# Performance work log

Hardware: AMD Instinct MI355X
Metric: run time of the kernel (lower is better)

Reference implementation:

```python
import jax, jax.numpy as jnp
import numpy as np

B = 16384
D = 64            # bottom_mlp_layers[-1] = embedding_dim
DENSE = 512
HIST = 50         # history length per row
C_CAMP = 1000     # num_collisions for campaign table (sqrt(1e6))
C_FEAT = 316      # num_collisions for 1e5-vocab tables
NQ_CAMP = 1000    # ceil(1e6/1000)
NQ_FEAT = 317     # ceil(1e5/316)
NFEAT = 7
N = NFEAT + 1 + 1 # sparse features + dense row
PROJ = 128


def setup_inputs() -> dict:
    key = jax.random.key(0)
    ks = jax.random.split(key, 20)
    inp = {
        'x': jax.random.normal(ks[0], (B, DENSE), jnp.float32),
        'hist_idx': jax.random.randint(ks[1], (B * HIST,), 0, 1000000),
        'hist_offsets': jnp.arange(B, dtype=jnp.int64) * HIST,
        'feat_idx': jax.random.randint(ks[2], (B, NFEAT), 0, 100000),
        # QR embedding tables (quotient, remainder)
        'Wq_c': jax.random.normal(ks[3], (NQ_CAMP, D), jnp.float32) * 0.05,
        'Wr_c': jax.random.normal(ks[4], (C_CAMP, D), jnp.float32) * 0.05,
        'Wq_f': jax.random.normal(ks[5], (NFEAT, NQ_FEAT, D), jnp.float32) * 0.05,
        'Wr_f': jax.random.normal(ks[6], (NFEAT, C_FEAT, D), jnp.float32) * 0.05,
        # bottom MLP: 512->512 relu 512->256 relu 256->64
        'W0': jax.random.normal(ks[7], (512, DENSE), jnp.float32) * 0.03,
        'b0': jnp.zeros((512,), jnp.float32),
        'W1': jax.random.normal(ks[8], (256, 512), jnp.float32) * 0.04,
        'b1': jnp.zeros((256,), jnp.float32),
        'W2': jax.random.normal(ks[9], (64, 256), jnp.float32) * 0.06,
        'b2': jnp.zeros((64,), jnp.float32),
        # projection: (D + (N^2-N)/2) -> PROJ ; 64 + 36 = 100
        'Wp': jax.random.normal(ks[10], (PROJ, D + (N * N - N) // 2), jnp.float32) * 0.1,
        'bp': jnp.zeros((PROJ,), jnp.float32),
    }
    return inp


def _forward(x, hist_idx, hist_offsets, feat_idx, Wq_c, Wr_c, Wq_f, Wr_f,
             W0, b0, W1, b1, W2, b2, Wp, bp):
    # bottom MLP
    h = jax.nn.relu(x @ W0.T + b0)
    h = jax.nn.relu(h @ W1.T + b1)
    dense = h @ W2.T + b2                                   # [B, D]

    # QR embedding bag (mode='mean', operation='mult') for history feature
    e = Wq_c[hist_idx // C_CAMP] * Wr_c[hist_idx % C_CAMP]  # [M, D]
    M = hist_idx.shape[0]
    seg = jnp.cumsum(jnp.zeros((M,), jnp.int32).at[hist_offsets].add(1)) - 1
    sums = jax.ops.segment_sum(e, seg, num_segments=B)      # [B, D]
    counts = jnp.diff(jnp.concatenate([hist_offsets, jnp.array([M], hist_offsets.dtype)]))
    hist_emb = sums / counts[:, None].astype(sums.dtype)

    # single-valued QR lookups (bag size 1 -> mean == lookup)
    t = jnp.arange(NFEAT)[None, :]
    fe = Wq_f[t, feat_idx // C_FEAT] * Wr_f[t, feat_idx % C_FEAT]  # [B, NFEAT, D]

    # pairwise dot interaction: upper triangle (offset=1) of T @ T^T
    T = jnp.concatenate([dense[:, None, :], hist_emb[:, None, :], fe], axis=1)  # [B, N, D]
    Z = jnp.einsum('bnd,bmd->bnm', T, T)
    row, col = np.triu_indices(N, k=1)
    Z_flat = Z[:, row, col]                                  # [B, (N^2-N)/2]

    combined = jnp.concatenate([dense, Z_flat], axis=1)
    return combined @ Wp.T + bp                              # [B, PROJ]


def reference(x, hist_idx, hist_offsets, feat_idx, Wq_c, Wr_c, Wq_f, Wr_f,
              W0, b0, W1, b1, W2, b2, Wp, bp):
    return _forward(x, hist_idx, hist_offsets, feat_idx, Wq_c, Wr_c, Wq_f, Wr_f,
                    W0, b0, W1, b1, W2, b2, Wp, bp)
```

## Files before the change

### kernel.cpp

```cpp
#include <hip/hip_runtime.h>
#include <hip/hip_bf16.h>
#include <stdint.h>

#define DENSE_D 512
#define HIDDEN1 512
#define HIDDEN2 256
#define EMB_D   64
#define NFEAT   7
#define NROWS   9
#define NPAIRS  36
#define COMB    100
#define KPROJ   128
#define PROJ    128
#define C_CAMP  1000
#define C_FEAT  316
#define NQ_FEAT 317
#define TROWS   16

typedef __attribute__((ext_vector_type(8)))  __bf16 bf16x8;
typedef __attribute__((ext_vector_type(8)))  unsigned short ushort8;
typedef __attribute__((ext_vector_type(4)))  float  facc4;

#define GLD_LDS16(gp, lp) __builtin_amdgcn_global_load_lds( \
    (__attribute__((address_space(1))) void*)(gp), \
    (__attribute__((address_space(3))) void*)(lp), 16, 0, 0)

__device__ inline unsigned short f2bf(float f) {
    __hip_bfloat16 h = __float2bfloat16(f);
    return *reinterpret_cast<unsigned short*>(&h);
}
__device__ inline float blo(unsigned int u) { return __uint_as_float(u << 16); }
__device__ inline float bhi(unsigned int u) { return __uint_as_float(u & 0xffff0000u); }
__device__ inline unsigned int pack2(unsigned short lo, unsigned short hi) {
    return (unsigned int)lo | ((unsigned int)hi << 16);
}

template<int BM, int BN, int BK, int WM, int WN, bool RELU, bool A_F32>
__global__ __launch_bounds__(WM * WN * 64)
void gemm16(const void* __restrict__ Avoid,
            const unsigned short* __restrict__ W,
            const float* __restrict__ bias,
            unsigned short* __restrict__ Cout,
            int M, int N, int K)
{
    constexpr int THREADS = WM * WN * 64;
    constexpr int MREP    = BM / (WM * 16);
    constexpr int NREP    = BN / (WN * 16);
    constexpr int SUB     = BK / 32;
    constexpr int ACH     = BM * BK / 8;
    constexpr int BCH     = BN * BK / 8;

    __shared__ __align__(16) unsigned short Asm[BK / 8][BM][8];
    __shared__ __align__(16) unsigned short Bsm[BK / 8][BN][8];

    const int tid  = threadIdx.x;
    const int lane = tid & 63;
    const int wave = tid >> 6;
    const int wm   = wave / WN;
    const int wn   = wave % WN;
    const int row0 = blockIdx.x * BM;
    const int col0 = blockIdx.y * BN;
    const int fr   = lane & 15;
    const int fk   = lane >> 4;

    facc4 acc[MREP][NREP] = {};

    for (int k0 = 0; k0 < K; k0 += BK) {
        if (A_F32) {
            const float* Af = (const float*)Avoid;
            #pragma unroll
            for (int it = 0; it < ACH / THREADS; ++it) {
                const int p  = it * THREADS + tid;
                const int r  = p & (BM - 1);
                const int kc = p / BM;
                const float* src = Af + (size_t)(row0 + r) * K + k0 + kc * 8;
                const float4 v0 = *reinterpret_cast<const float4*>(src);
                const float4 v1 = *reinterpret_cast<const float4*>(src + 4);
                ushort8 cv;
                cv[0] = f2bf(v0.x); cv[1] = f2bf(v0.y);
                cv[2] = f2bf(v0.z); cv[3] = f2bf(v0.w);
                cv[4] = f2bf(v1.x); cv[5] = f2bf(v1.y);
                cv[6] = f2bf(v1.z); cv[7] = f2bf(v1.w);
                *reinterpret_cast<ushort8*>(
                    (unsigned short*)(&Asm[0][0][0]) + (size_t)p * 8) = cv;
            }
        } else {
            const unsigned short* Ab = (const unsigned short*)Avoid;
            #pragma unroll
            for (int it = 0; it < ACH / THREADS; ++it) {
                const int p  = it * THREADS + tid;
                const int r  = p & (BM - 1);
                const int kc = p / BM;
                GLD_LDS16(Ab + (size_t)(row0 + r) * K + k0 + kc * 8,
                          (&Asm[0][0][0]) + (size_t)p * 8);
            }
        }
        #pragma unroll
        for (int it = 0; it < BCH / THREADS; ++it) {
            const int p  = it * THREADS + tid;
            const int r  = p & (BN - 1);
            const int kc = p / BN;
            GLD_LDS16(W + (size_t)(col0 + r) * K + k0 + kc * 8,
                      (&Bsm[0][0][0]) + (size_t)p * 8);
        }
        __syncthreads();

        #pragma unroll
        for (int s = 0; s < SUB; ++s) {
            bf16x8 af[MREP], bw[NREP];
            #pragma unroll
            for (int m = 0; m < MREP; ++m)
                af[m] = *reinterpret_cast<const bf16x8*>(
                    &Asm[s * 4 + fk][wm * (MREP * 16) + m * 16 + fr][0]);
            #pragma unroll
            for (int n = 0; n < NREP; ++n)
                bw[n] = *reinterpret_cast<const bf16x8*>(
                    &Bsm[s * 4 + fk][wn * (NREP * 16) + n * 16 + fr][0]);
            #pragma unroll
            for (int m = 0; m < MREP; ++m)
                #pragma unroll
                for (int n = 0; n < NREP; ++n)
                    acc[m][n] = __builtin_amdgcn_mfma_f32_16x16x32_bf16(
                        af[m], bw[n], acc[m][n], 0, 0, 0);
        }
        __syncthreads();
    }

    #pragma unroll
    for (int n = 0; n < NREP; ++n) {
        const int col = col0 + wn * (NREP * 16) + n * 16 + fr;
        const float bv = bias[col];
        #pragma unroll
        for (int m = 0; m < MREP; ++m) {
            #pragma unroll
            for (int j = 0; j < 4; ++j) {
                const int row = row0 + wm * (MREP * 16) + m * 16 + fk * 4 + j;
                float v = acc[m][n][j] + bv;
                if (RELU) v = fmaxf(v, 0.f);
                Cout[(size_t)row * N + col] = f2bf(v);
            }
        }
    }
}

__device__ inline void cast_seg(const float* __restrict__ src,
                                unsigned short* __restrict__ dst,
                                int n4, int id, int stride)
{
    for (int i = id; i < n4; i += stride) {
        const float4 v = reinterpret_cast<const float4*>(src)[i];
        ushort4 o;
        o.x = f2bf(v.x); o.y = f2bf(v.y); o.z = f2bf(v.z); o.w = f2bf(v.w);
        reinterpret_cast<ushort4*>(dst)[i] = o;
    }
}

__global__ __launch_bounds__(256)
void prep_all(const float* __restrict__ W0, const float* __restrict__ W1,
              const float* __restrict__ W2, const float* __restrict__ Wp,
              const float* __restrict__ Wq_c, const float* __restrict__ Wr_c,
              const float* __restrict__ Wq_f, const float* __restrict__ Wr_f,
              unsigned short* w0b, unsigned short* w1b, unsigned short* w2b,
              unsigned short* wpb, unsigned short* qcb, unsigned short* rcb,
              unsigned short* qfb, unsigned short* rfb)
{
    const int id = blockIdx.x * blockDim.x + threadIdx.x;
    const int stride = gridDim.x * blockDim.x;
    cast_seg(W0,   w0b, HIDDEN1 * DENSE_D / 4,   id, stride);
    cast_seg(W1,   w1b, HIDDEN2 * HIDDEN1 / 4,   id, stride);
    cast_seg(W2,   w2b, EMB_D * HIDDEN2 / 4,     id, stride);
    cast_seg(Wq_c, qcb, C_CAMP * EMB_D / 4,      id, stride);
    cast_seg(Wr_c, rcb, C_CAMP * EMB_D / 4,      id, stride);
    cast_seg(Wq_f, qfb, NFEAT * NQ_FEAT * EMB_D / 4, id, stride);
    cast_seg(Wr_f, rfb, NFEAT * C_FEAT * EMB_D / 4,  id, stride);
    for (int i = id; i < PROJ * KPROJ; i += stride) {
        const int r = i >> 7, c = i & 127;
        wpb[i] = (c < COMB) ? f2bf(Wp[r * COMB + c]) : (unsigned short)0;
    }
}

__global__ __launch_bounds__(1024)
void tail_fused(const unsigned short* __restrict__ h1b,
                const unsigned short* __restrict__ w2b,
                const float* __restrict__ b2,
                const int* __restrict__ hist_idx,
                const int* __restrict__ hist_off,
                const int* __restrict__ feat_idx,
                const unsigned short* __restrict__ qcb,
                const unsigned short* __restrict__ rcb,
                const unsigned short* __restrict__ qfb,
                const unsigned short* __restrict__ rfb,
                const unsigned short* __restrict__ wpb,
                const float* __restrict__ bp,
                float* __restrict__ out,
                int B, int Mtot)
{
    const int r0   = blockIdx.x * TROWS;
    const int t    = threadIdx.x;
    const int lane = t & 63;
    const int wave = t >> 6;
    const int fr   = lane & 15;
    const int fk   = lane >> 4;

    __shared__ __align__(16) unsigned short T[TROWS][NROWS][68];
    __shared__ __align__(16) unsigned short combs[TROWS][136];

    if (wave < 4) {
        facc4 acc = {};
        const unsigned short* arow = h1b + (size_t)(r0 + fr) * HIDDEN2;
        const unsigned short* brow = w2b + (size_t)(wave * 16 + fr) * HIDDEN2;
        #pragma unroll
        for (int kw = 0; kw < 8; ++kw) {
            const bf16x8 af = *reinterpret_cast<const bf16x8*>(arow + kw * 32 + fk * 8);
            const bf16x8 bw = *reinterpret_cast<const bf16x8*>(brow + kw * 32 + fk * 8);
            acc = __builtin_amdgcn_mfma_f32_16x16x32_bf16(af, bw, acc, 0, 0, 0);
        }
        const int col = wave * 16 + fr;
        const float bv = b2[col];
        #pragma unroll
        for (int j = 0; j < 4; ++j) {
            const int row = fk * 4 + j;
            const unsigned short hv = f2bf(acc[j] + bv);
            T[row][0][col]  = hv;
            combs[row][col] = hv;
        }
    }

    for (int p = t; p < TROWS * 18; p += 1024) {
        const int row = p / 18, c = p % 18;
        *reinterpret_cast<unsigned int*>(&combs[row][100 + c * 2]) = 0u;
    }

    {
        const int row = wave;
        const int br  = r0 + row;
        const int h   = lane >> 5;
        const int l2  = lane & 31;

        #pragma unroll
        for (int j = 0; j < 4; ++j) {
            const int f = h * 4 + j;
            if (f < NFEAT) {
                const int fi = feat_idx[br * NFEAT + f];
                const int q = fi / C_FEAT, r = fi - q * C_FEAT;
                const unsigned int qv = *reinterpret_cast<const unsigned int*>(
                    qfb + ((size_t)f * NQ_FEAT + q) * EMB_D + 2 * l2);
                const unsigned int rv = *reinterpret_cast<const unsigned int*>(
                    rfb + ((size_t)f * C_FEAT + r) * EMB_D + 2 * l2);
                *reinterpret_cast<unsigned int*>(&T[row][2 + f][2 * l2]) =
                    pack2(f2bf(blo(qv) * blo(rv)), f2bf(bhi(qv) * bhi(rv)));
            }
        }

        const int start = hist_off[br];
        const int end   = (br + 1 < B) ? hist_off[br + 1] : Mtot;
        const int cnt   = end - start;
        int qo = 0, ro = 0;
        if (lane < cnt) {
            const int hi = hist_idx[start + lane];
            const int qq = hi / C_CAMP;
            qo = qq * EMB_D;
            ro = (hi - qq * C_CAMP) * EMB_D;
        }

        float a0 = 0.f, a1 = 0.f;
        const int nit = (cnt + 1) >> 1;
        for (int i = 0; i < nit; ++i) {
            const int idx = 2 * i + h;
            const int qoi = __shfl(qo, idx);
            const int roi = __shfl(ro, idx);
            const unsigned int uq = *reinterpret_cast<const unsigned int*>(
                qcb + qoi + 2 * l2);
            const unsigned int ur = *reinterpret_cast<const unsigned int*>(
                rcb + roi + 2 * l2);
            if (idx < cnt) {
                a0 += blo(uq) * blo(ur);
                a1 += bhi(uq) * bhi(ur);
            }
        }
        a0 += __shfl_xor(a0, 32);
        a1 += __shfl_xor(a1, 32);
        if (h == 0) {
            const float inv = 1.f / (float)max(cnt, 1);
            *reinterpret_cast<unsigned int*>(&T[row][1][2 * l2]) =
                pack2(f2bf(a0 * inv), f2bf(a1 * inv));
        }
    }
    __syncthreads();

    for (int p = t; p < NPAIRS * TROWS; p += 1024) {
        const int row = p & (TROWS - 1);
        const int pr  = p / TROWS;
        int i = 0, rem = pr;
        while (rem >= (NROWS - 1) - i) { rem -= (NROWS - 1) - i; ++i; }
        const int j = i + 1 + rem;
        const unsigned short* ti = &T[row][i][0];
        const unsigned short* tj = &T[row][j][0];
        float s = 0.f;
        #pragma unroll
        for (int d = 0; d < EMB_D; d += 4) {
            const uint2 u = *reinterpret_cast<const uint2*>(ti + d);
            const uint2 v = *reinterpret_cast<const uint2*>(tj + d);
            s += blo(u.x) * blo(v.x) + bhi(u.x) * bhi(v.x)
               + blo(u.y) * blo(v.y) + bhi(u.y) * bhi(v.y);
        }
        combs[row][EMB_D + pr] = f2bf(s);
    }
    __syncthreads();

    if (wave < 8) {
        facc4 acc = {};
        #pragma unroll
        for (int kw = 0; kw < 4; ++kw) {
            const bf16x8 af = *reinterpret_cast<const bf16x8*>(
                &combs[fr][kw * 32 + fk * 8]);
            const bf16x8 bw = *reinterpret_cast<const bf16x8*>(
                wpb + (size_t)(wave * 16 + fr) * KPROJ + kw * 32 + fk * 8);
            acc = __builtin_amdgcn_mfma_f32_16x16x32_bf16(af, bw, acc, 0, 0, 0);
        }
        const int col = wave * 16 + fr;
        const float bv = bp[col];
        #pragma unroll
        for (int j = 0; j < 4; ++j) {
            const int row = fk * 4 + j;
            out[(size_t)(r0 + row) * PROJ + col] = acc[j] + bv;
        }
    }
}

extern "C" void kernel_launch(void* const* d_in, const int* in_sizes, int n_in,
                              void* d_out, int out_size, void* d_ws, size_t ws_size,
                              hipStream_t stream)
{
    const float* x        = (const float*)d_in[0];
    const int*   hist_idx = (const int*)  d_in[1];
    const int*   hist_off = (const int*)  d_in[2];
    const int*   feat_idx = (const int*)  d_in[3];
    const float* Wq_c     = (const float*)d_in[4];
    const float* Wr_c     = (const float*)d_in[5];
    const float* Wq_f     = (const float*)d_in[6];
    const float* Wr_f     = (const float*)d_in[7];
    const float* W0       = (const float*)d_in[8];
    const float* b0       = (const float*)d_in[9];
    const float* W1       = (const float*)d_in[10];
    const float* b1       = (const float*)d_in[11];
    const float* W2       = (const float*)d_in[12];
    const float* b2       = (const float*)d_in[13];
    const float* Wp       = (const float*)d_in[14];
    const float* bp       = (const float*)d_in[15];

    const int M    = in_sizes[0] / DENSE_D;
    const int Mtot = in_sizes[1];

    char* w = (char*)d_ws;
    auto take = [&](size_t bytes) { char* p = w; w += (bytes + 255) & ~(size_t)255; return p; };
    unsigned short* w0b = (unsigned short*)take(HIDDEN1 * DENSE_D * 2);
    unsigned short* w1b = (unsigned short*)take(HIDDEN2 * HIDDEN1 * 2);
    unsigned short* w2b = (unsigned short*)take(EMB_D * HIDDEN2 * 2);
    unsigned short* wpb = (unsigned short*)take(PROJ * KPROJ * 2);
    unsigned short* qcb = (unsigned short*)take(C_CAMP * EMB_D * 2);
    unsigned short* rcb = (unsigned short*)take(C_CAMP * EMB_D * 2);
    unsigned short* qfb = (unsigned short*)take(NFEAT * NQ_FEAT * EMB_D * 2);
    unsigned short* rfb = (unsigned short*)take(NFEAT * C_FEAT * EMB_D * 2);
    unsigned short* h0b = (unsigned short*)take((size_t)M * HIDDEN1 * 2);
    unsigned short* h1b = (unsigned short*)take((size_t)M * HIDDEN2 * 2);

    prep_all<<<256, 256, 0, stream>>>(W0, W1, W2, Wp, Wq_c, Wr_c, Wq_f, Wr_f,
                                      w0b, w1b, w2b, wpb, qcb, rcb, qfb, rfb);

    gemm16<128, 128, 32, 2, 2, true, true>
        <<<dim3(M / 128, HIDDEN1 / 128), 256, 0, stream>>>(
        x, w0b, b0, h0b, M, HIDDEN1, DENSE_D);

    gemm16<64, 128, 64, 1, 4, true, false>
        <<<dim3(M / 64, HIDDEN2 / 128), 256, 0, stream>>>(
        h0b, w1b, b1, h1b, M, HIDDEN2, HIDDEN1);

    tail_fused<<<M / TROWS, 1024, 0, stream>>>(
        h1b, w2b, b2, hist_idx, hist_off, feat_idx,
        qcb, rcb, qfb, rfb, wpb, bp, (float*)d_out, M, Mtot);
}
```

Baseline: 88.52 us.

## Halve tail block rows to 8 and gather four history items per wave step

The fused tail kernel now processes 8 rows per block with 512 threads instead of 16 rows with 1024. Its MFMA tiles are padded so rows 8-15 duplicate rows 0-7, and only the valid half is written. The history embedding-bag loop now has each 16-lane quarter-wave handle one item, with each lane loading 4 bf16 values, so four items are processed per iteration instead of two. The partial sums are then reduced across the quarters with shuffles. Smaller blocks should improve occupancy and load balance, at the cost of wasting half of each MFMA and of more blocks overall.

```diff
diff --git a/kernel.cpp b/kernel.cpp
--- a/kernel.cpp
+++ b/kernel.cpp
@@ -15,7 +15,7 @@
 #define C_CAMP  1000
 #define C_FEAT  316
 #define NQ_FEAT 317
-#define TROWS   16
+#define TROWS   8
 
 typedef __attribute__((ext_vector_type(8)))  __bf16 bf16x8;
 typedef __attribute__((ext_vector_type(8)))  unsigned short ushort8;
@@ -179,7 +179,7 @@
     }
 }
 
-__global__ __launch_bounds__(1024)
+__global__ __launch_bounds__(512)
 void tail_fused(const unsigned short* __restrict__ h1b,
                 const unsigned short* __restrict__ w2b,
                 const float* __restrict__ b2,
@@ -207,7 +207,7 @@
 
     if (wave < 4) {
         facc4 acc = {};
-        const unsigned short* arow = h1b + (size_t)(r0 + fr) * HIDDEN2;
+        const unsigned short* arow = h1b + (size_t)(r0 + (fr & 7)) * HIDDEN2;
         const unsigned short* brow = w2b + (size_t)(wave * 16 + fr) * HIDDEN2;
         #pragma unroll
         for (int kw = 0; kw < 8; ++kw) {
@@ -215,18 +215,20 @@
             const bf16x8 bw = *reinterpret_cast<const bf16x8*>(brow + kw * 32 + fk * 8);
             acc = __builtin_amdgcn_mfma_f32_16x16x32_bf16(af, bw, acc, 0, 0, 0);
         }
-        const int col = wave * 16 + fr;
-        const float bv = b2[col];
-        #pragma unroll
-        for (int j = 0; j < 4; ++j) {
-            const int row = fk * 4 + j;
-            const unsigned short hv = f2bf(acc[j] + bv);
-            T[row][0][col]  = hv;
-            combs[row][col] = hv;
-        }
-    }
-
-    for (int p = t; p < TROWS * 18; p += 1024) {
+        if (fk < 2) {
+            const int col = wave * 16 + fr;
+            const float bv = b2[col];
+            #pragma unroll
+            for (int j = 0; j < 4; ++j) {
+                const int row = fk * 4 + j;
+                const unsigned short hv = f2bf(acc[j] + bv);
+                T[row][0][col]  = hv;
+                combs[row][col] = hv;
+            }
+        }
+    }
+
+    for (int p = t; p < TROWS * 18; p += 512) {
         const int row = p / 18, c = p % 18;
         *reinterpret_cast<unsigned int*>(&combs[row][100 + c * 2]) = 0u;
     }
@@ -234,12 +236,12 @@
     {
         const int row = wave;
         const int br  = r0 + row;
-        const int h   = lane >> 5;
+        const int h2  = lane >> 5;
         const int l2  = lane & 31;
 
         #pragma unroll
         for (int j = 0; j < 4; ++j) {
-            const int f = h * 4 + j;
+            const int f = h2 * 4 + j;
             if (f < NFEAT) {
                 const int fi = feat_idx[br * NFEAT + f];
                 const int q = fi / C_FEAT, r = fi - q * C_FEAT;
@@ -263,32 +265,52 @@
             ro = (hi - qq * C_CAMP) * EMB_D;
         }
 
-        float a0 = 0.f, a1 = 0.f;
-        const int nit = (cnt + 1) >> 1;
-        for (int i = 0; i < nit; ++i) {
-            const int idx = 2 * i + h;
+        const int h4 = lane >> 4;
+        const int l4 = lane & 15;
+        const unsigned short* qb = qcb + l4 * 4;
+        const unsigned short* rb = rcb + l4 * 4;
+        float a0 = 0.f, a1 = 0.f, a2 = 0.f, a3 = 0.f;
+        const int ngrp = cnt >> 2;
+        #pragma unroll 4
+        for (int g = 0; g < ngrp; ++g) {
+            const int idx = g * 4 + h4;
             const int qoi = __shfl(qo, idx);
             const int roi = __shfl(ro, idx);
-            const unsigned int uq = *reinterpret_cast<const unsigned int*>(
-                qcb + qoi + 2 * l2);
-            const unsigned int ur = *reinterpret_cast<const unsigned int*>(
-                rcb + roi + 2 * l2);
+            const uint2 uq = *reinterpret_cast<const uint2*>(qb + qoi);
+            const uint2 ur = *reinterpret_cast<const uint2*>(rb + roi);
+            a0 += blo(uq.x) * blo(ur.x);
+            a1 += bhi(uq.x) * bhi(ur.x);
+            a2 += blo(uq.y) * blo(ur.y);
+            a3 += bhi(uq.y) * bhi(ur.y);
+        }
+        {
+            const int idx = (ngrp << 2) + h4;
+            const int qoi = __shfl(qo, idx & 63);
+            const int roi = __shfl(ro, idx & 63);
+            const uint2 uq = *reinterpret_cast<const uint2*>(qb + qoi);
+            const uint2 ur = *reinterpret_cast<const uint2*>(rb + roi);
             if (idx < cnt) {
-                a0 += blo(uq) * blo(ur);
-                a1 += bhi(uq) * bhi(ur);
-            }
-        }
-        a0 += __shfl_xor(a0, 32);
-        a1 += __shfl_xor(a1, 32);
-        if (h == 0) {
+                a0 += blo(uq.x) * blo(ur.x);
+                a1 += bhi(uq.x) * bhi(ur.x);
+                a2 += blo(uq.y) * blo(ur.y);
+                a3 += bhi(uq.y) * bhi(ur.y);
+            }
+        }
+        a0 += __shfl_xor(a0, 16); a1 += __shfl_xor(a1, 16);
+        a2 += __shfl_xor(a2, 16); a3 += __shfl_xor(a3, 16);
+        a0 += __shfl_xor(a0, 32); a1 += __shfl_xor(a1, 32);
+        a2 += __shfl_xor(a2, 32); a3 += __shfl_xor(a3, 32);
+        if (lane < 16) {
             const float inv = 1.f / (float)max(cnt, 1);
-            *reinterpret_cast<unsigned int*>(&T[row][1][2 * l2]) =
-                pack2(f2bf(a0 * inv), f2bf(a1 * inv));
+            uint2 o;
+            o.x = pack2(f2bf(a0 * inv), f2bf(a1 * inv));
+            o.y = pack2(f2bf(a2 * inv), f2bf(a3 * inv));
+            *reinterpret_cast<uint2*>(&T[row][1][l4 * 4]) = o;
         }
     }
     __syncthreads();
 
-    for (int p = t; p < NPAIRS * TROWS; p += 1024) {
+    for (int p = t; p < NPAIRS * TROWS; p += 512) {
         const int row = p & (TROWS - 1);
         const int pr  = p / TROWS;
         int i = 0, rem = pr;
@@ -308,22 +330,24 @@
     }
     __syncthreads();
 
-    if (wave < 8) {
+    {
         facc4 acc = {};
         #pragma unroll
         for (int kw = 0; kw < 4; ++kw) {
             const bf16x8 af = *reinterpret_cast<const bf16x8*>(
-                &combs[fr][kw * 32 + fk * 8]);
+                &combs[fr & 7][kw * 32 + fk * 8]);
             const bf16x8 bw = *reinterpret_cast<const bf16x8*>(
                 wpb + (size_t)(wave * 16 + fr) * KPROJ + kw * 32 + fk * 8);
             acc = __builtin_amdgcn_mfma_f32_16x16x32_bf16(af, bw, acc, 0, 0, 0);
         }
-        const int col = wave * 16 + fr;
-        const float bv = bp[col];
-        #pragma unroll
-        for (int j = 0; j < 4; ++j) {
-            const int row = fk * 4 + j;
-            out[(size_t)(r0 + row) * PROJ + col] = acc[j] + bv;
+        if (fk < 2) {
+            const int col = wave * 16 + fr;
+            const float bv = bp[col];
+            #pragma unroll
+            for (int j = 0; j < 4; ++j) {
+                const int row = fk * 4 + j;
+                out[(size_t)(r0 + row) * PROJ + col] = acc[j] + bv;
+            }
         }
     }
 }
@@ -376,7 +400,7 @@
         <<<dim3(M / 64, HIDDEN2 / 128), 256, 0, stream>>>(
         h0b, w1b, b1, h1b, M, HIDDEN2, HIDDEN1);
 
-    tail_fused<<<M / TROWS, 1024, 0, stream>>>(
+    tail_fused<<<M / TROWS, 512, 0, stream>>>(
         h1b, w2b, b2, hist_idx, hist_off, feat_idx,
         qcb, rcb, qfb, rfb, wpb, bp, (float*)d_out, M, Mtot);
 }
```

After: 94.70 us. 1.07x slower.
